# Performance work log

Hardware: AMD Instinct MI355X
Metric: run time of the kernel (lower is better)

## Reference

```python
import jax, jax.numpy as jnp
import numpy as np

N = 4096
D_IN = 1024
D_Q = 1024
D_V = 1024

def setup_inputs() -> dict:
    key = jax.random.key(0)
    ks = jax.random.split(key, 8)
    # x scaled down a bit so exp() of raw (unstable, no max-subtract) scores stays finite,
    # matching the original module's numerics regime.
    x = jax.random.normal(ks[0], (N, D_IN), dtype=jnp.float32) * 0.02
    mask = jax.random.uniform(ks[1], (N, N), dtype=jnp.float32)
    s = 1.0 / np.sqrt(D_IN)
    Wq = jax.random.normal(ks[2], (D_IN, D_Q), dtype=jnp.float32) * s
    bq = jax.random.normal(ks[3], (D_Q,), dtype=jnp.float32) * 0.02
    Wk = jax.random.normal(ks[4], (D_IN, D_Q), dtype=jnp.float32) * s
    bk = jax.random.normal(ks[5], (D_Q,), dtype=jnp.float32) * 0.02
    Wv = jax.random.normal(ks[6], (D_IN, D_V), dtype=jnp.float32) * s
    bv = jax.random.normal(ks[7], (D_V,), dtype=jnp.float32) * 0.02
    return {"x": x, "mask": mask, "Wq": Wq, "bq": bq, "Wk": Wk, "bk": bk, "Wv": Wv, "bv": bv}

def reference(x, mask, Wq, bq, Wk, bk, Wv, bv):
    # Q, K, V projections (nn.Linear: x @ W + b, here W stored as [in, out])
    Q = x @ Wq + bq          # [N, Dq]
    K = x @ Wk + bk          # [N, Dq]
    V = x @ Wv + bv          # [N, Dv]
    scale = 1.0              # default scale in original forward
    scores = scale * (Q @ K.T)   # [N, N]
    scores = mask * scores       # elementwise multiplicative mask
    # Faithful to original (quirky) normalization:
    # exp(S) / sum(exp(S), axis=1)[None, :]  -> row-sums broadcast across ROWS
    e = jnp.exp(scores)                       # [N, N]
    denom = jnp.sum(e, axis=1)[None, :]       # [1, N]
    softmax = e / denom                       # [N, N]
    return softmax @ V                        # [N, Dv]
```

## Files before the change

kernel.cpp:

```cpp
#include <hip/hip_runtime.h>
#include <hip/hip_bf16.h>


#define N_TOK 4096
#define D_DIM 1024
#define VS_SCALE 131072.0f

typedef __bf16 bf16x8 __attribute__((ext_vector_type(8)));
typedef __bf16 bf16x4 __attribute__((ext_vector_type(4)));
typedef float  f32x4  __attribute__((ext_vector_type(4)));

typedef const __attribute__((address_space(1))) char g_char;
typedef __attribute__((address_space(3))) char lds_char;

__device__ inline unsigned char f32_to_fp8(float f) {
    return (unsigned char)(__builtin_amdgcn_cvt_pk_fp8_f32(f, f, 0, false) & 0xff);
}

__global__ void cvt_and_bias(const float* __restrict__ x, __bf16* __restrict__ xb,
                             const float* __restrict__ bq, const float* __restrict__ bk,
                             const float* __restrict__ bv, float* __restrict__ bcat) {
    int b = blockIdx.x;
    if (b < 4096) {
        int i = (b * 256 + threadIdx.x) * 4;
        float4 v = *(const float4*)(x + i);
        bf16x4 o;
        o.x = (__bf16)v.x; o.y = (__bf16)v.y;
        o.z = (__bf16)v.z; o.w = (__bf16)v.w;
        *(bf16x4*)(xb + i) = o;
    } else {
        int i = (b - 4096) * 256 + threadIdx.x;
        if (i < 1024) bcat[i] = bq[i];
        else if (i < 2048) bcat[i] = bk[i - 1024];
        else if (i < 3072) bcat[i] = bv[i - 2048];
    }
}

__global__ void transpose_w3(const float* __restrict__ Wq, const float* __restrict__ Wk,
                             const float* __restrict__ Wv, __bf16* __restrict__ outT) {
    const float* in = (blockIdx.z == 0) ? Wq : (blockIdx.z == 1) ? Wk : Wv;
    __bf16* oT = outT + (size_t)blockIdx.z * 1024 * 1024;
    __shared__ float t[64][65];
    const int c0 = blockIdx.x * 64, r0 = blockIdx.y * 64;
    const int tid = threadIdx.x;
#pragma unroll
    for (int k = 0; k < 16; k++) {
        int lin = tid + k * 256;
        int r = lin >> 6, c = lin & 63;
        t[r][c] = in[(size_t)(r0 + r) * 1024 + c0 + c];
    }
    __syncthreads();
#pragma unroll
    for (int k = 0; k < 16; k++) {
        int lin = tid + k * 256;
        int c = lin >> 6, r = lin & 63;
        oT[(size_t)(c0 + c) * 1024 + r0 + r] = (__bf16)t[r][c];
    }
}

__global__ void scale_transpose(const __bf16* __restrict__ V, int ldv,
                                const float* __restrict__ denom,
                                unsigned char* __restrict__ VT8) {
    __shared__ float t[64][65];
    __shared__ float rd[64];
    const int d0 = blockIdx.x * 64, j0 = blockIdx.y * 64;
    const int tid = threadIdx.x;
    if (tid < 64) rd[tid] = VS_SCALE / denom[j0 + tid];
    __syncthreads();
#pragma unroll
    for (int k = 0; k < 16; k++) {
        int lin = tid + k * 256;
        int j = lin >> 6, d = lin & 63;
        t[j][d] = (float)V[(size_t)(j0 + j) * ldv + d0 + d] * rd[j];
    }
    __syncthreads();
#pragma unroll
    for (int k = 0; k < 16; k++) {
        int lin = tid + k * 256;
        int d = lin >> 6, j = lin & 63;
        VT8[(size_t)(d0 + d) * N_TOK + j0 + j] = f32_to_fp8(t[j][d]);
    }
}

template <int EPI>
__global__ __launch_bounds__(512, 2)
void gemm_nt_256(const __bf16* __restrict__ A, const __bf16* __restrict__ B,
                 int lda, int ldb, int ldc, int K,
                 const float* __restrict__ bias,
                 const float* __restrict__ mask,
                 __bf16* __restrict__ Cb, unsigned char* __restrict__ C8,
                 float* __restrict__ denom) {
    __shared__ __bf16 ldsb[4 * 16384];

    const int tid  = threadIdx.x;
    const int wave = tid >> 6;
    const int lane = tid & 63;
    const int quad = lane >> 4;
    const int l16  = lane & 15;

    const int nbx = gridDim.x;
    const int nwg = gridDim.x * gridDim.y;
    const int bid = blockIdx.y * nbx + blockIdx.x;
    const int cpx = nwg >> 3;
    const int swz = (bid & 7) * cpx + (bid >> 3);
    const int m0 = (swz / nbx) * 256;
    const int n0 = (swz % nbx) * 256;

    const int wr = (wave >> 2) * 128;
    const int wc = (wave & 3) * 64;

    const size_t lda_b = (size_t)lda * 2;
    const size_t ldb_b = (size_t)ldb * 2;
    const int trow = tid >> 2;
    const int tcs  = ((tid & 3) ^ ((tid >> 3) & 3)) * 16;
    const char* gA = (const char*)A + (size_t)(m0 + trow) * lda_b + tcs;
    const char* gB = (const char*)B + (size_t)(n0 + trow) * ldb_b + tcs;
    const size_t rstepA = 128 * lda_b;
    const size_t rstepB = 128 * ldb_b;

    lds_char* lw = (lds_char*)(void*)ldsb + tid * 16;

    const int cswz = (quad ^ ((l16 >> 1) & 3)) * 16;
    const int aOff = (wr + l16) * 64 + cswz;
    const int bOff = (wc + l16) * 64 + cswz + 16384;

    f32x4 acc[8][4];
#pragma unroll
    for (int i = 0; i < 8; i++)
#pragma unroll
        for (int j = 0; j < 4; j++) acc[i][j] = (f32x4){0.f, 0.f, 0.f, 0.f};

    const int H = K >> 5;

#define STAGEH(hh) do {                                                              \
    const char* ga_ = gA + (size_t)(hh) * 64;                                        \
    const char* gb_ = gB + (size_t)(hh) * 64;                                        \
    lds_char* ls_ = lw + ((hh) & 3) * 32768;                                         \
    __builtin_amdgcn_global_load_lds((g_char*)(ga_),          ls_,          16, 0, 0); \
    __builtin_amdgcn_global_load_lds((g_char*)(ga_ + rstepA), ls_ + 8192,   16, 0, 0); \
    __builtin_amdgcn_global_load_lds((g_char*)(gb_),          ls_ + 16384,  16, 0, 0); \
    __builtin_amdgcn_global_load_lds((g_char*)(gb_ + rstepB), ls_ + 24576,  16, 0, 0); \
} while (0)

    STAGEH(0);
    STAGEH(1);
    STAGEH(2);

    for (int h = 0; h < H; ++h) {
        if (h + 2 < H)      asm volatile("s_waitcnt vmcnt(8)" ::: "memory");
        else if (h + 1 < H) asm volatile("s_waitcnt vmcnt(4)" ::: "memory");
        else                asm volatile("s_waitcnt vmcnt(0)" ::: "memory");
        __builtin_amdgcn_s_barrier();
        __builtin_amdgcn_sched_barrier(0);
        if (h + 3 < H) STAGEH(h + 3);

        const char* sb = (const char*)ldsb + (h & 3) * 32768;
        bf16x8 af[8], bfr[4];
#pragma unroll
        for (int i = 0; i < 8; i++) af[i] = *(const bf16x8*)(sb + aOff + i * 1024);
#pragma unroll
        for (int j = 0; j < 4; j++) bfr[j] = *(const bf16x8*)(sb + bOff + j * 1024);

        __builtin_amdgcn_s_setprio(1);
#pragma unroll
        for (int i = 0; i < 8; i++)
#pragma unroll
            for (int j = 0; j < 4; j++)
                acc[i][j] = __builtin_amdgcn_mfma_f32_16x16x32_bf16(
                    af[i], bfr[j], acc[i][j], 0, 0, 0);
        __builtin_amdgcn_s_setprio(0);
        __builtin_amdgcn_sched_barrier(0);
    }
#undef STAGEH

#pragma unroll
    for (int i = 0; i < 8; i++) {
        const int rbase = m0 + wr + i * 16 + quad * 4;
        f32x4 rs = (f32x4){0.f, 0.f, 0.f, 0.f};
#pragma unroll
        for (int j = 0; j < 4; j++) {
            const int col = n0 + wc + j * 16 + l16;
            f32x4 v = acc[i][j];
            if (EPI == 0) {
                const float bb = bias[col];
#pragma unroll
                for (int r = 0; r < 4; r++)
                    Cb[(size_t)(rbase + r) * ldc + col] = (__bf16)(v[r] + bb);
            } else {
#pragma unroll
                for (int r = 0; r < 4; r++) {
                    size_t idx = (size_t)(rbase + r) * ldc + col;
                    float e = __expf(mask[idx] * v[r]);
                    C8[idx] = f32_to_fp8(e);
                    rs[r] += e;
                }
            }
        }
        if (EPI == 1) {
#pragma unroll
            for (int m = 1; m < 16; m <<= 1) {
#pragma unroll
                for (int r = 0; r < 4; r++) rs[r] += __shfl_xor(rs[r], m, 64);
            }
            if (l16 == 0) {
#pragma unroll
                for (int r = 0; r < 4; r++) atomicAdd(&denom[rbase + r], rs[r]);
            }
        }
    }
}

__global__ __launch_bounds__(256, 2)
void gemm_out_fp8(const unsigned char* __restrict__ A,
                  const unsigned char* __restrict__ B,
                  float* __restrict__ C) {
    __shared__ unsigned char lA[128 * 128];
    __shared__ unsigned char lB[64 * 128];

    const int tid  = threadIdx.x;
    const int wave = tid >> 6;
    const int lane = tid & 63;
    const int quad = lane >> 4;
    const int l16  = lane & 15;
    const int m0 = blockIdx.y * 128;
    const int n0 = blockIdx.x * 64;
    const int wr = (wave >> 1) * 64;
    const int wc = (wave & 1) * 32;

    const int tr = tid >> 3;
    const int ts = ((tid & 7) ^ (tr & 7)) * 16;
    const char* gA = (const char*)A + (size_t)(m0 + tr) * N_TOK + ts;
    const char* gB = (const char*)B + (size_t)(n0 + tr) * N_TOK + ts;
    const size_t pstep = (size_t)32 * N_TOK;

    lds_char* lAp = (lds_char*)(void*)lA + wave * 1024;
    lds_char* lBp = (lds_char*)(void*)lB + wave * 1024;

    const int l7 = l16 & 7;
    const int qhi = quad >> 1, qlo = (quad & 1) * 8;
    int rdA[4], rdB[4];
#pragma unroll
    for (int k = 0; k < 4; k++) {
        rdA[k] = ((k * 2 + qhi) ^ l7) * 16 + qlo;
        rdB[k] = rdA[k];
    }

    f32x4 acc[4][2];
#pragma unroll
    for (int i = 0; i < 4; i++)
#pragma unroll
        for (int j = 0; j < 2; j++) acc[i][j] = (f32x4){0.f, 0.f, 0.f, 0.f};

    for (int kt = 0; kt < N_TOK; kt += 128) {
#pragma unroll
        for (int c = 0; c < 4; c++)
            __builtin_amdgcn_global_load_lds((g_char*)(gA + c * pstep),
                                             lAp + c * 4096, 16, 0, 0);
#pragma unroll
        for (int c = 0; c < 2; c++)
            __builtin_amdgcn_global_load_lds((g_char*)(gB + c * pstep),
                                             lBp + c * 4096, 16, 0, 0);
        gA += 128;
        gB += 128;
        __syncthreads();

#pragma unroll
        for (int k = 0; k < 4; k++) {
            long a[4], b[2];
#pragma unroll
            for (int i = 0; i < 4; i++)
                a[i] = *(const long*)&lA[(wr + i * 16 + l16) * 128 + rdA[k]];
#pragma unroll
            for (int j = 0; j < 2; j++)
                b[j] = *(const long*)&lB[(wc + j * 16 + l16) * 128 + rdB[k]];
#pragma unroll
            for (int i = 0; i < 4; i++)
#pragma unroll
                for (int j = 0; j < 2; j++)
                    acc[i][j] = __builtin_amdgcn_mfma_f32_16x16x32_fp8_fp8(
                        a[i], b[j], acc[i][j], 0, 0, 0);
        }
        __syncthreads();
    }

#pragma unroll
    for (int i = 0; i < 4; i++) {
#pragma unroll
        for (int j = 0; j < 2; j++) {
            const int col   = n0 + wc + j * 16 + l16;
            const int rbase = m0 + wr + i * 16 + quad * 4;
            f32x4 v = acc[i][j];
#pragma unroll
            for (int r = 0; r < 4; r++)
                C[(size_t)(rbase + r) * D_DIM + col] = v[r] * (1.0f / VS_SCALE);
        }
    }
}

extern "C" void kernel_launch(void* const* d_in, const int* in_sizes, int n_in,
                              void* d_out, int out_size, void* d_ws, size_t ws_size,
                              hipStream_t stream) {
    const float* x    = (const float*)d_in[0];
    const float* mask = (const float*)d_in[1];
    const float* Wq   = (const float*)d_in[2];
    const float* bq   = (const float*)d_in[3];
    const float* Wk   = (const float*)d_in[4];
    const float* bk   = (const float*)d_in[5];
    const float* Wv   = (const float*)d_in[6];
    const float* bv   = (const float*)d_in[7];
    float* out = (float*)d_out;
    char* ws = (char*)d_ws;

    const size_t MB = 1024 * 1024;
    unsigned char* E8   = (unsigned char*)(ws + 0 * MB);
    __bf16* QKVb  = (__bf16*)(ws + 16 * MB);
    __bf16* xb    = (__bf16*)(ws + 40 * MB);
    unsigned char* VsT8 = (unsigned char*)xb;
    __bf16* WcatT = (__bf16*)(ws + 48 * MB);
    float*  bcat  = (float*)(ws + 54 * MB);
    float*  denom = (float*)(ws + 54 * MB + 64 * 1024);

    hipMemsetAsync(denom, 0, N_TOK * sizeof(float), stream);

    cvt_and_bias<<<4096 + 12, 256, 0, stream>>>(x, xb, bq, bk, bv, bcat);
    transpose_w3<<<dim3(16, 16, 3), 256, 0, stream>>>(Wq, Wk, Wv, WcatT);

    gemm_nt_256<0><<<dim3(12, 16), 512, 0, stream>>>(
        xb, WcatT, D_DIM, D_DIM, 3 * D_DIM, D_DIM,
        bcat, nullptr, QKVb, nullptr, nullptr);

    const __bf16* Qb = QKVb;
    const __bf16* Kb = QKVb + D_DIM;
    gemm_nt_256<1><<<dim3(16, 16), 512, 0, stream>>>(
        Qb, Kb, 3 * D_DIM, 3 * D_DIM, N_TOK, D_DIM,
        nullptr, mask, nullptr, E8, denom);

    scale_transpose<<<dim3(16, 64), 256, 0, stream>>>(QKVb + 2048, 3 * D_DIM, denom, VsT8);

    gemm_out_fp8<<<dim3(16, 32), 256, 0, stream>>>(E8, VsT8, out);
}
```

Before: 249.6 us.

## Restructure GEMM mainloop into 4-phase ping-pong with 64-wide K tiles

Replaces the 4-stage, 32-wide-K cp.async-style pipeline with a double-buffered 64-wide-K tile scheme, split into four compute phases per tile. Each phase interleaves a slice of global->LDS staging and fragment loads with MFMA bursts, bracketed by barriers and priority changes. Launch bounds drop from 2 to 1 block per CU to allow more registers for prefetched fragments. The aim is better overlap of memory and matrix work and fewer barriers per K step. The cost is lower occupancy and more frequent block-wide barriers.

Result: no change. 251.7 us (+0.8%).

```diff
diff --git a/kernel.cpp b/kernel.cpp
--- a/kernel.cpp
+++ b/kernel.cpp
@@ -83,20 +83,21 @@
 }
 
 template <int EPI>
-__global__ __launch_bounds__(512, 2)
+__global__ __launch_bounds__(512, 1)
 void gemm_nt_256(const __bf16* __restrict__ A, const __bf16* __restrict__ B,
                  int lda, int ldb, int ldc, int K,
                  const float* __restrict__ bias,
                  const float* __restrict__ mask,
                  __bf16* __restrict__ Cb, unsigned char* __restrict__ C8,
                  float* __restrict__ denom) {
-    __shared__ __bf16 ldsb[4 * 16384];
+    __shared__ __bf16 ldsb[2 * 32768];
 
     const int tid  = threadIdx.x;
     const int wave = tid >> 6;
     const int lane = tid & 63;
     const int quad = lane >> 4;
     const int l16  = lane & 15;
+    const int l7   = l16 & 7;
 
     const int nbx = gridDim.x;
     const int nwg = gridDim.x * gridDim.y;
@@ -106,23 +107,30 @@
     const int m0 = (swz / nbx) * 256;
     const int n0 = (swz % nbx) * 256;
 
-    const int wr = (wave >> 2) * 128;
+    const int wg = wave >> 2;
+    const int wr = wg * 128;
     const int wc = (wave & 3) * 64;
 
     const size_t lda_b = (size_t)lda * 2;
     const size_t ldb_b = (size_t)ldb * 2;
-    const int trow = tid >> 2;
-    const int tcs  = ((tid & 3) ^ ((tid >> 3) & 3)) * 16;
-    const char* gA = (const char*)A + (size_t)(m0 + trow) * lda_b + tcs;
-    const char* gB = (const char*)B + (size_t)(n0 + trow) * ldb_b + tcs;
-    const size_t rstepA = 128 * lda_b;
-    const size_t rstepB = 128 * ldb_b;
-
-    lds_char* lw = (lds_char*)(void*)ldsb + tid * 16;
-
-    const int cswz = (quad ^ ((l16 >> 1) & 3)) * 16;
-    const int aOff = (wr + l16) * 64 + cswz;
-    const int bOff = (wc + l16) * 64 + cswz + 16384;
+    const int trow  = tid >> 3;
+    const int base0 = (trow & 31) | ((trow & 32) << 1);
+    const int cg    = ((tid & 7) ^ (trow & 7)) * 16;
+    const char* gAt = (const char*)A + (size_t)(m0 + base0) * lda_b + cg;
+    const char* gBt = (const char*)B + (size_t)(n0 + base0) * ldb_b + cg;
+    const size_t a32 = (size_t)32 * lda_b,  a128 = (size_t)128 * lda_b;
+    const size_t b32 = (size_t)32 * ldb_b,  b128 = (size_t)128 * ldb_b;
+
+    lds_char* lwA = (lds_char*)(void*)ldsb + tid * 16;
+    lds_char* lwB = lwA + 32768;
+
+    const int cs0 = (quad ^ l7) * 16;
+    const int cs1 = ((4 + quad) ^ l7) * 16;
+    const int aRowB = (wg * 64 + l16) * 128;
+    const int bRowB = 32768 + ((wc >> 6) * 32 + l16) * 128;
+
+#define AOFF(i) (((i >> 1) & 1) * 16384 + aRowB + (((i >> 2) * 32 + ((i) & 1) * 16) * 128))
+#define BOFF(j) ((((j) >> 1) & 1) * 16384 + bRowB + ((((j) & 1) * 16) * 128))
 
     f32x4 acc[8][4];
 #pragma unroll
@@ -130,48 +138,114 @@
 #pragma unroll
         for (int j = 0; j < 4; j++) acc[i][j] = (f32x4){0.f, 0.f, 0.f, 0.f};
 
-    const int H = K >> 5;
-
-#define STAGEH(hh) do {                                                              \
-    const char* ga_ = gA + (size_t)(hh) * 64;                                        \
-    const char* gb_ = gB + (size_t)(hh) * 64;                                        \
-    lds_char* ls_ = lw + ((hh) & 3) * 32768;                                         \
-    __builtin_amdgcn_global_load_lds((g_char*)(ga_),          ls_,          16, 0, 0); \
-    __builtin_amdgcn_global_load_lds((g_char*)(ga_ + rstepA), ls_ + 8192,   16, 0, 0); \
-    __builtin_amdgcn_global_load_lds((g_char*)(gb_),          ls_ + 16384,  16, 0, 0); \
-    __builtin_amdgcn_global_load_lds((g_char*)(gb_ + rstepB), ls_ + 24576,  16, 0, 0); \
+    bf16x8 aA[2][2], aB[2][2], bfr[4][2];
+
+    const int NT = K >> 6;
+    const char* lbase = (const char*)(const void*)ldsb;
+
+#define STG_A(h, tt, dd) do {                                                        \
+    const char* ga_ = gAt + (size_t)(h) * a32 + (size_t)(tt) * 128;                  \
+    lds_char* l_ = lwA + (dd) * 65536 + (h) * 16384;                                 \
+    __builtin_amdgcn_global_load_lds((g_char*)ga_,          l_,        16, 0, 0);    \
+    __builtin_amdgcn_global_load_lds((g_char*)(ga_ + a128), l_ + 8192, 16, 0, 0);    \
 } while (0)
-
-    STAGEH(0);
-    STAGEH(1);
-    STAGEH(2);
-
-    for (int h = 0; h < H; ++h) {
-        if (h + 2 < H)      asm volatile("s_waitcnt vmcnt(8)" ::: "memory");
-        else if (h + 1 < H) asm volatile("s_waitcnt vmcnt(4)" ::: "memory");
-        else                asm volatile("s_waitcnt vmcnt(0)" ::: "memory");
-        __builtin_amdgcn_s_barrier();
-        __builtin_amdgcn_sched_barrier(0);
-        if (h + 3 < H) STAGEH(h + 3);
-
-        const char* sb = (const char*)ldsb + (h & 3) * 32768;
-        bf16x8 af[8], bfr[4];
-#pragma unroll
-        for (int i = 0; i < 8; i++) af[i] = *(const bf16x8*)(sb + aOff + i * 1024);
-#pragma unroll
-        for (int j = 0; j < 4; j++) bfr[j] = *(const bf16x8*)(sb + bOff + j * 1024);
-
-        __builtin_amdgcn_s_setprio(1);
-#pragma unroll
-        for (int i = 0; i < 8; i++)
-#pragma unroll
-            for (int j = 0; j < 4; j++)
-                acc[i][j] = __builtin_amdgcn_mfma_f32_16x16x32_bf16(
-                    af[i], bfr[j], acc[i][j], 0, 0, 0);
-        __builtin_amdgcn_s_setprio(0);
-        __builtin_amdgcn_sched_barrier(0);
-    }
-#undef STAGEH
+#define STG_B(h, tt, dd) do {                                                        \
+    const char* gb_ = gBt + (size_t)(h) * b32 + (size_t)(tt) * 128;                  \
+    lds_char* l_ = lwB + (dd) * 65536 + (h) * 16384;                                 \
+    __builtin_amdgcn_global_load_lds((g_char*)gb_,          l_,        16, 0, 0);    \
+    __builtin_amdgcn_global_load_lds((g_char*)(gb_ + b128), l_ + 8192, 16, 0, 0);    \
+} while (0)
+
+#define LDA2(dst, f0, f1, SB) do {                                                   \
+    dst[0][0] = *(const bf16x8*)((SB) + AOFF(f0) + cs0);                             \
+    dst[0][1] = *(const bf16x8*)((SB) + AOFF(f0) + cs1);                             \
+    dst[1][0] = *(const bf16x8*)((SB) + AOFF(f1) + cs0);                             \
+    dst[1][1] = *(const bf16x8*)((SB) + AOFF(f1) + cs1);                             \
+} while (0)
+#define LDB_ALL(SB) do {                                                             \
+    _Pragma("unroll")                                                                \
+    for (int j = 0; j < 4; j++) {                                                    \
+        bfr[j][0] = *(const bf16x8*)((SB) + BOFF(j) + cs0);                          \
+        bfr[j][1] = *(const bf16x8*)((SB) + BOFF(j) + cs1);                          \
+    }                                                                                \
+} while (0)
+#define MF_QUAD(q, aX) do {                                                          \
+    _Pragma("unroll")                                                                \
+    for (int ii = 0; ii < 2; ii++)                                                   \
+    _Pragma("unroll")                                                                \
+    for (int j = 0; j < 4; j++) {                                                    \
+        acc[2*(q)+ii][j] = __builtin_amdgcn_mfma_f32_16x16x32_bf16(                  \
+            aX[ii][0], bfr[j][0], acc[2*(q)+ii][j], 0, 0, 0);                        \
+        acc[2*(q)+ii][j] = __builtin_amdgcn_mfma_f32_16x16x32_bf16(                  \
+            aX[ii][1], bfr[j][1], acc[2*(q)+ii][j], 0, 0, 0);                        \
+    }                                                                                \
+} while (0)
+#define PHASE_SYNC_PRE()  do { __builtin_amdgcn_s_barrier();                         \
+    asm volatile("s_waitcnt lgkmcnt(0)" ::: "memory");                               \
+    __builtin_amdgcn_sched_barrier(0);                                               \
+    __builtin_amdgcn_s_setprio(1); } while (0)
+#define PHASE_SYNC_POST() do { __builtin_amdgcn_s_setprio(0);                        \
+    __builtin_amdgcn_sched_barrier(0);                                               \
+    __builtin_amdgcn_s_barrier(); } while (0)
+
+    STG_B(1, 0, 0);
+    STG_A(0, 0, 0);
+    STG_B(0, 0, 0);
+    STG_A(1, 0, 0);
+    asm volatile("s_waitcnt vmcnt(0)" ::: "memory");
+    __builtin_amdgcn_s_barrier();
+    LDA2(aA, 0, 1, lbase);
+
+    for (int t = 0; t < NT; ++t) {
+        const int d = t & 1;
+        const char* sb  = lbase + d * 65536;
+        const char* sbn = lbase + (d ^ 1) * 65536;
+        const int dn = d ^ 1;
+        const int tn = t + 1;
+        const bool pf = (tn < NT);
+
+        if (pf) {
+            STG_B(1, tn, dn);
+            asm volatile("s_waitcnt vmcnt(2)" ::: "memory");
+        } else {
+            asm volatile("s_waitcnt vmcnt(0)" ::: "memory");
+        }
+        LDB_ALL(sb);
+        LDA2(aB, 2, 3, sb);
+        PHASE_SYNC_PRE();
+        MF_QUAD(0, aA);
+        PHASE_SYNC_POST();
+
+        if (pf) STG_A(0, tn, dn);
+        LDA2(aA, 4, 5, sb);
+        PHASE_SYNC_PRE();
+        MF_QUAD(1, aB);
+        PHASE_SYNC_POST();
+
+        if (pf) STG_B(0, tn, dn);
+        LDA2(aB, 6, 7, sb);
+        PHASE_SYNC_PRE();
+        MF_QUAD(2, aA);
+        PHASE_SYNC_POST();
+
+        if (pf) {
+            STG_A(1, tn, dn);
+            asm volatile("s_waitcnt vmcnt(2)" ::: "memory");
+            LDA2(aA, 0, 1, sbn);
+        }
+        PHASE_SYNC_PRE();
+        MF_QUAD(3, aB);
+        PHASE_SYNC_POST();
+    }
+#undef STG_A
+#undef STG_B
+#undef LDA2
+#undef LDB_ALL
+#undef MF_QUAD
+#undef PHASE_SYNC_PRE
+#undef PHASE_SYNC_POST
+#undef AOFF
+#undef BOFF
 
 #pragma unroll
     for (int i = 0; i < 8; i++) {
```

## Double-buffer A fragments in registers and software-pipeline mask loads in QK^T epilogue

Applied to the files above, without the earlier changes.

The main GEMM loop is unrolled by two, with A fragments ping-ponged between two register sets so LDS reads for the next K-step overlap the current step's MFMAs. lgkmcnt waits are placed explicitly. The QK^T epilogue now prefetches mask rows two row-blocks ahead in a ping-pong pattern to hide global load latency behind the exp, fp8 and atomic work. Launch bounds change from 2 to 1 waves-per-EU to give the extra registers room, which lowers occupancy.

New measurement: 248.8 us. No clear change (-0.3%).

```diff
diff --git a/kernel.cpp b/kernel.cpp
--- a/kernel.cpp
+++ b/kernel.cpp
@@ -83,13 +83,13 @@
 }
 
 template <int EPI>
-__global__ __launch_bounds__(512, 2)
-void gemm_nt_256(const __bf16* __restrict__ A, const __bf16* __restrict__ B,
-                 int lda, int ldb, int ldc, int K,
-                 const float* __restrict__ bias,
-                 const float* __restrict__ mask,
-                 __bf16* __restrict__ Cb, unsigned char* __restrict__ C8,
-                 float* __restrict__ denom) {
+__device__ __forceinline__
+void gemm_nt_body(const __bf16* __restrict__ A, const __bf16* __restrict__ B,
+                  int lda, int ldb, int ldc, int K,
+                  const float* __restrict__ bias,
+                  const float* __restrict__ mask,
+                  __bf16* __restrict__ Cb, unsigned char* __restrict__ C8,
+                  float* __restrict__ denom) {
     __shared__ __bf16 ldsb[4 * 16384];
 
     const int tid  = threadIdx.x;
@@ -131,6 +131,9 @@
         for (int j = 0; j < 4; j++) acc[i][j] = (f32x4){0.f, 0.f, 0.f, 0.f};
 
     const int H = K >> 5;
+    const char* lbase = (const char*)(const void*)ldsb;
+
+    bf16x8 a0[8], a1[8], bC[4];
 
 #define STAGEH(hh) do {                                                              \
     const char* ga_ = gA + (size_t)(hh) * 64;                                        \
@@ -142,72 +145,150 @@
     __builtin_amdgcn_global_load_lds((g_char*)(gb_ + rstepB), ls_ + 24576,  16, 0, 0); \
 } while (0)
 
+#define READ_A8(AV, slot) do {                                                       \
+    const char* sb_ = lbase + (slot) * 32768;                                        \
+    _Pragma("unroll")                                                                \
+    for (int i_ = 0; i_ < 8; i_++)                                                   \
+        AV[i_] = *(const bf16x8*)(sb_ + aOff + i_ * 1024);                           \
+} while (0)
+
+#define READ_B4(slot) do {                                                           \
+    const char* sb_ = lbase + (slot) * 32768;                                        \
+    _Pragma("unroll")                                                                \
+    for (int j_ = 0; j_ < 4; j_++)                                                   \
+        bC[j_] = *(const bf16x8*)(sb_ + bOff + j_ * 1024);                           \
+} while (0)
+
+#define MFMA32(AU) do {                                                              \
+    _Pragma("unroll")                                                                \
+    for (int i_ = 0; i_ < 8; i_++)                                                   \
+    _Pragma("unroll")                                                                \
+    for (int j_ = 0; j_ < 4; j_++)                                                   \
+        acc[i_][j_] = __builtin_amdgcn_mfma_f32_16x16x32_bf16(                       \
+            AU[i_], bC[j_], acc[i_][j_], 0, 0, 0);                                   \
+} while (0)
+
+#define PHASE(hh, AU, AV) do {                                                       \
+    const bool pf1_ = (hh) + 1 < H;                                                  \
+    const bool pf2_ = (hh) + 2 < H;                                                  \
+    if (pf1_) {                                                                      \
+        if (pf2_) asm volatile("s_waitcnt vmcnt(4)" ::: "memory");                   \
+        else      asm volatile("s_waitcnt vmcnt(0)" ::: "memory");                   \
+    }                                                                                \
+    __builtin_amdgcn_s_barrier();                                                    \
+    if ((hh) + 3 < H) STAGEH((hh) + 3);                                              \
+    READ_B4((hh) & 3);                                                               \
+    if (pf1_) READ_A8(AV, ((hh) + 1) & 3);                                           \
+    if (pf1_) asm volatile("s_waitcnt lgkmcnt(8)" ::: "memory");                     \
+    else      asm volatile("s_waitcnt lgkmcnt(0)" ::: "memory");                     \
+    __builtin_amdgcn_sched_barrier(0);                                               \
+    __builtin_amdgcn_s_setprio(1);                                                   \
+    MFMA32(AU);                                                                      \
+    __builtin_amdgcn_s_setprio(0);                                                   \
+    __builtin_amdgcn_sched_barrier(0);                                               \
+} while (0)
+
     STAGEH(0);
     STAGEH(1);
     STAGEH(2);
-
-    for (int h = 0; h < H; ++h) {
-        if (h + 2 < H)      asm volatile("s_waitcnt vmcnt(8)" ::: "memory");
-        else if (h + 1 < H) asm volatile("s_waitcnt vmcnt(4)" ::: "memory");
-        else                asm volatile("s_waitcnt vmcnt(0)" ::: "memory");
-        __builtin_amdgcn_s_barrier();
-        __builtin_amdgcn_sched_barrier(0);
-        if (h + 3 < H) STAGEH(h + 3);
-
-        const char* sb = (const char*)ldsb + (h & 3) * 32768;
-        bf16x8 af[8], bfr[4];
-#pragma unroll
-        for (int i = 0; i < 8; i++) af[i] = *(const bf16x8*)(sb + aOff + i * 1024);
-#pragma unroll
-        for (int j = 0; j < 4; j++) bfr[j] = *(const bf16x8*)(sb + bOff + j * 1024);
-
-        __builtin_amdgcn_s_setprio(1);
-#pragma unroll
-        for (int i = 0; i < 8; i++)
-#pragma unroll
-            for (int j = 0; j < 4; j++)
-                acc[i][j] = __builtin_amdgcn_mfma_f32_16x16x32_bf16(
-                    af[i], bfr[j], acc[i][j], 0, 0, 0);
-        __builtin_amdgcn_s_setprio(0);
-        __builtin_amdgcn_sched_barrier(0);
+    asm volatile("s_waitcnt vmcnt(8)" ::: "memory");
+    __builtin_amdgcn_s_barrier();
+    READ_A8(a0, 0);
+
+    for (int h0 = 0; h0 < H; h0 += 2) {
+        PHASE(h0,     a0, a1);
+        PHASE(h0 + 1, a1, a0);
     }
 #undef STAGEH
-
-#pragma unroll
-    for (int i = 0; i < 8; i++) {
-        const int rbase = m0 + wr + i * 16 + quad * 4;
-        f32x4 rs = (f32x4){0.f, 0.f, 0.f, 0.f};
-#pragma unroll
-        for (int j = 0; j < 4; j++) {
-            const int col = n0 + wc + j * 16 + l16;
-            f32x4 v = acc[i][j];
-            if (EPI == 0) {
+#undef READ_A8
+#undef READ_B4
+#undef MFMA32
+#undef PHASE
+
+    if (EPI == 0) {
+#pragma unroll
+        for (int i = 0; i < 8; i++) {
+            const int rbase = m0 + wr + i * 16 + quad * 4;
+#pragma unroll
+            for (int j = 0; j < 4; j++) {
+                const int col = n0 + wc + j * 16 + l16;
+                f32x4 v = acc[i][j];
                 const float bb = bias[col];
 #pragma unroll
                 for (int r = 0; r < 4; r++)
                     Cb[(size_t)(rbase + r) * ldc + col] = (__bf16)(v[r] + bb);
-            } else {
-#pragma unroll
-                for (int r = 0; r < 4; r++) {
-                    size_t idx = (size_t)(rbase + r) * ldc + col;
-                    float e = __expf(mask[idx] * v[r]);
-                    C8[idx] = f32_to_fp8(e);
-                    rs[r] += e;
-                }
             }
         }
-        if (EPI == 1) {
-#pragma unroll
-            for (int m = 1; m < 16; m <<= 1) {
-#pragma unroll
-                for (int r = 0; r < 4; r++) rs[r] += __shfl_xor(rs[r], m, 64);
-            }
-            if (l16 == 0) {
-#pragma unroll
-                for (int r = 0; r < 4; r++) atomicAdd(&denom[rbase + r], rs[r]);
-            }
-        }
-    }
+    } else {
+        const float* mrow = mask + (size_t)(m0 + wr + quad * 4) * (size_t)ldc
+                            + (n0 + wc + l16);
+        unsigned char* crow = C8 + (size_t)(m0 + wr + quad * 4) * (size_t)ldc
+                            + (n0 + wc + l16);
+        float mk0[4][4], mk1[4][4];
+#define LOADC(dst, ii) do {                                                         \
+    _Pragma("unroll")                                                               \
+    for (int j = 0; j < 4; j++)                                                     \
+    _Pragma("unroll")                                                               \
+    for (int r = 0; r < 4; r++)                                                     \
+        dst[j][r] = mrow[(size_t)((ii) * 16 + r) * (size_t)ldc + j * 16];           \
+} while (0)
+#define CONSUME(ii, mk) do {                                                        \
+    f32x4 rs = (f32x4){0.f, 0.f, 0.f, 0.f};                                         \
+    _Pragma("unroll")                                                               \
+    for (int j = 0; j < 4; j++) {                                                   \
+        f32x4 v = acc[ii][j];                                                       \
+        _Pragma("unroll")                                                           \
+        for (int r = 0; r < 4; r++) {                                               \
+            float e = __expf(mk[j][r] * v[r]);                                      \
+            crow[(size_t)((ii) * 16 + r) * (size_t)ldc + j * 16] = f32_to_fp8(e);   \
+            rs[r] += e;                                                             \
+        }                                                                           \
+    }                                                                               \
+    _Pragma("unroll")                                                               \
+    for (int m = 1; m < 16; m <<= 1)                                                \
+        _Pragma("unroll")                                                           \
+        for (int r = 0; r < 4; r++) rs[r] += __shfl_xor(rs[r], m, 64);              \
+    if (l16 == 0) {                                                                 \
+        const int rb = m0 + wr + (ii) * 16 + quad * 4;                              \
+        _Pragma("unroll")                                                           \
+        for (int r = 0; r < 4; r++) atomicAdd(&denom[rb + r], rs[r]);               \
+    }                                                                               \
+} while (0)
+        LOADC(mk0, 0);
+        LOADC(mk1, 1);
+        CONSUME(0, mk0); __builtin_amdgcn_sched_barrier(0);
+        LOADC(mk0, 2);
+        CONSUME(1, mk1); __builtin_amdgcn_sched_barrier(0);
+        LOADC(mk1, 3);
+        CONSUME(2, mk0); __builtin_amdgcn_sched_barrier(0);
+        LOADC(mk0, 4);
+        CONSUME(3, mk1); __builtin_amdgcn_sched_barrier(0);
+        LOADC(mk1, 5);
+        CONSUME(4, mk0); __builtin_amdgcn_sched_barrier(0);
+        LOADC(mk0, 6);
+        CONSUME(5, mk1); __builtin_amdgcn_sched_barrier(0);
+        LOADC(mk1, 7);
+        CONSUME(6, mk0); __builtin_amdgcn_sched_barrier(0);
+        CONSUME(7, mk1);
+#undef LOADC
+#undef CONSUME
+    }
+}
+
+__global__ __launch_bounds__(512, 1)
+void gemm_qkv(const __bf16* __restrict__ A, const __bf16* __restrict__ B,
+              int lda, int ldb, int ldc, int K,
+              const float* __restrict__ bias,
+              __bf16* __restrict__ Cb) {
+    gemm_nt_body<0>(A, B, lda, ldb, ldc, K, bias, nullptr, Cb, nullptr, nullptr);
+}
+
+__global__ __launch_bounds__(512, 1)
+void gemm_qkt(const __bf16* __restrict__ A, const __bf16* __restrict__ B,
+              int lda, int ldb, int ldc, int K,
+              const float* __restrict__ mask,
+              unsigned char* __restrict__ C8, float* __restrict__ denom) {
+    gemm_nt_body<1>(A, B, lda, ldb, ldc, K, nullptr, mask, nullptr, C8, denom);
 }
 
 __global__ __launch_bounds__(256, 2)
@@ -325,15 +406,13 @@
     cvt_and_bias<<<4096 + 12, 256, 0, stream>>>(x, xb, bq, bk, bv, bcat);
     transpose_w3<<<dim3(16, 16, 3), 256, 0, stream>>>(Wq, Wk, Wv, WcatT);
 
-    gemm_nt_256<0><<<dim3(12, 16), 512, 0, stream>>>(
-        xb, WcatT, D_DIM, D_DIM, 3 * D_DIM, D_DIM,
-        bcat, nullptr, QKVb, nullptr, nullptr);
+    gemm_qkv<<<dim3(12, 16), 512, 0, stream>>>(
+        xb, WcatT, D_DIM, D_DIM, 3 * D_DIM, D_DIM, bcat, QKVb);
 
     const __bf16* Qb = QKVb;
     const __bf16* Kb = QKVb + D_DIM;
-    gemm_nt_256<1><<<dim3(16, 16), 512, 0, stream>>>(
-        Qb, Kb, 3 * D_DIM, 3 * D_DIM, N_TOK, D_DIM,
-        nullptr, mask, nullptr, E8, denom);
+    gemm_qkt<<<dim3(16, 16), 512, 0, stream>>>(
+        Qb, Kb, 3 * D_DIM, 3 * D_DIM, N_TOK, D_DIM, mask, E8, denom);
 
     scale_transpose<<<dim3(16, 64), 256, 0, stream>>>(QKVb + 2048, 3 * D_DIM, denom, VsT8);
 
```
